# Optimization experiments

Measured on AMD Instinct MI355X. Metric: run time of the kernel, lower is better.

Reference implementation:

```python
import jax, jax.numpy as jnp
import numpy as np


def setup_inputs() -> dict:
    key = jax.random.key(0)
    kq, kk, kv, km = jax.random.split(key, 4)
    B, H, S, D = 1, 16, 2048, 64
    q = jax.random.normal(kq, (B, H, S, D), dtype=jnp.float32)
    k = jax.random.normal(kk, (B, H, S, D), dtype=jnp.float32)
    v = jax.random.normal(kv, (B, H, S, D), dtype=jnp.float32)
    # Boolean attention mask: True = attend, False = ignore.
    # block-pruned use case while keeping the same dense-mask semantics.
    BLK = 64
    tile = jax.random.bernoulli(km, 0.5, (B, H, S // BLK, S // BLK))
    mask = jnp.repeat(jnp.repeat(tile, BLK, axis=2), BLK, axis=3)
    # Guarantee at least something per row is allowed in most rows is not
    # required: fully-masked rows legitimately produce zero output.
    return {"q": q, "k": k, "v": v, "mask": mask}


def reference(q, k, v, mask):
    # Masked scaled-dot-product attention; rows with no valid keys output 0,
    # matching the kernel's `acc / l_i if l_i > 0 else 0` behavior.
    D = q.shape[-1]
    scale = 1.0 / jnp.sqrt(jnp.asarray(D, q.dtype))
    qk = jnp.einsum("bhqd,bhkd->bhqk", q, k) * scale          # [B,H,S,S]
    neg_inf = jnp.asarray(-jnp.inf, qk.dtype)
    s = jnp.where(mask, qk, neg_inf)
    m = jnp.max(s, axis=-1, keepdims=True)                      # row max (may be -inf)
    m_safe = jnp.where(jnp.isfinite(m), m, jnp.zeros_like(m))
    p = jnp.where(mask, jnp.exp(s - m_safe), jnp.zeros_like(qk))  # unnormalized probs
    l = jnp.sum(p, axis=-1, keepdims=True)                      # [B,H,S,1]
    acc = jnp.einsum("bhqk,bhkd->bhqd", p, v)
    out = jnp.where(l > 0, acc / jnp.where(l > 0, l, jnp.ones_like(l)), jnp.zeros_like(acc))
    return out
```

## Files before the change

### kernel.cpp

```cpp
#include <hip/hip_runtime.h>
#include <hip/hip_bf16.h>
#include <stdint.h>

typedef __bf16 bf16;
typedef __attribute__((ext_vector_type(4))) __bf16 bf16x4;
typedef __attribute__((ext_vector_type(8))) __bf16 bf16x8;
typedef __attribute__((ext_vector_type(4))) float f32x4;
typedef __attribute__((ext_vector_type(4))) unsigned int u32x4;

#define NH 16
#define SEQ 2048
#define DH 64
#define NT 32
#define SCALE 0.125f
#define NEGINF (-1e30f)
#define IMG_TILE 8192

#define WS_KIMG  65536
#define WS_VIMG  (WS_KIMG + (size_t)NH * NT * IMG_TILE)
#define WS_NEED  (WS_VIMG + (size_t)NH * NT * IMG_TILE)

__device__ __forceinline__ unsigned swz16(int row, int bytecol) {
  return (unsigned)(row * 128 + (bytecol ^ ((row & 7) << 4)));
}

__global__ void __launch_bounds__(256) conv_kernel(
    const float* __restrict__ kg, const float* __restrict__ vg,
    unsigned char* __restrict__ ws)
{
  const int b = blockIdx.x, tid = threadIdx.x;
  const int h = b & 15, kt = b >> 4, kb = kt << 6;
  unsigned char* kimg = ws + WS_KIMG + (size_t)(h * NT + kt) * IMG_TILE;
  unsigned char* vimg = ws + WS_VIMG + (size_t)(h * NT + kt) * IMG_TILE;
  __shared__ float T[64][65];
  const int row = tid >> 2, c0 = (tid & 3) * 16;

  {
    const f32x4* rp = (const f32x4*)(kg + ((size_t)(h * SEQ) + kb + row) * DH + c0);
    f32x4 a0 = rp[0], a1 = rp[1], a2 = rp[2], a3 = rp[3];
    float* d = &T[row][c0];
    #pragma unroll
    for (int j = 0; j < 4; ++j) {
      d[j] = a0[j]; d[4 + j] = a1[j]; d[8 + j] = a2[j]; d[12 + j] = a3[j];
    }
  }
  __syncthreads();
  #pragma unroll
  for (int i = 0; i < 2; ++i) {
    const int slot = tid + 256 * i, g = slot >> 6, ll = slot & 63;
    const int nd = g >> 1, ks = g & 1;
    const float* s = &T[16 * nd + (ll & 15)][ks * 32 + (ll >> 4) * 8];
    bf16x8 o;
    #pragma unroll
    for (int j = 0; j < 8; ++j) o[j] = (bf16)s[j];
    *(bf16x8*)(kimg + slot * 16) = o;
  }
  __syncthreads();
  {
    const f32x4* rp = (const f32x4*)(vg + ((size_t)(h * SEQ) + kb + row) * DH + c0);
    f32x4 a0 = rp[0], a1 = rp[1], a2 = rp[2], a3 = rp[3];
    float* d = &T[row][c0];
    #pragma unroll
    for (int j = 0; j < 4; ++j) {
      d[j] = a0[j]; d[4 + j] = a1[j]; d[8 + j] = a2[j]; d[12 + j] = a3[j];
    }
  }
  __syncthreads();
  #pragma unroll
  for (int i = 0; i < 2; ++i) {
    const int slot = tid + 256 * i, g = slot >> 6, ll = slot & 63;
    const int nd = g >> 1, ks = g & 1;
    const int r0 = ks * 32 + (ll >> 4) * 8, col = 16 * nd + (ll & 15);
    bf16x8 o;
    #pragma unroll
    for (int j = 0; j < 8; ++j) o[j] = (bf16)T[r0 + j][col];
    *(bf16x8*)(vimg + slot * 16) = o;
  }
}

template<bool IMG>
__global__ void __launch_bounds__(256, 2) fused_attn_kernel(
    const float* __restrict__ qg, const float* __restrict__ kg,
    const float* __restrict__ vg, const void* __restrict__ maskg,
    float* __restrict__ outg, const unsigned char* __restrict__ ws)
{
  const int bid = blockIdx.x;
  const int h = bid & 15, qt = bid >> 4, qb = qt << 6;
  const int tid = threadIdx.x, l = tid & 63, rw = tid >> 6;
  const int qrow = l & 15, kgrp = l >> 4;

  __shared__ __attribute__((aligned(16))) bf16 Pl[4][1024];
  __shared__ unsigned sOr[2][32], sAnd[2][32];
  __shared__ unsigned char tfl[32];
  __shared__ unsigned char Ll[32];
  __shared__ int lcnt;
  __shared__ int clsS;

  bf16x8 qa[2];
  {
    const float* qp = qg + ((size_t)(h * SEQ) + qb + 16 * rw + qrow) * DH;
    #pragma unroll
    for (int ks = 0; ks < 2; ++ks) {
      f32x4 x0 = *(const f32x4*)(qp + ks * 32 + kgrp * 8);
      f32x4 x1 = *(const f32x4*)(qp + ks * 32 + kgrp * 8 + 4);
      bf16x8 a;
      #pragma unroll
      for (int j = 0; j < 4; ++j) {
        a[j] = (bf16)(x0[j] * SCALE); a[4 + j] = (bf16)(x1[j] * SCALE);
      }
      qa[ks] = a;
    }
  }

  if (tid == 0) clsS = 0;
  __syncthreads();
  {
    u32x4 t = ((const u32x4*)maskg)[tid];
    int bits = 0;
    #pragma unroll
    for (int j = 0; j < 4; ++j) {
      if (t[j] == 0x01010101u) bits |= 1;
      else if (t[j] == 1u) bits |= 2;
    }
    const int wb = (__any(bits & 1) ? 1 : 0) | (__any(bits & 2) ? 2 : 0);
    if (l == 0 && wb) atomicOr(&clsS, wb);
  }
  __syncthreads();
  const int byteMode = ((clsS & 1) || !(clsS & 2)) ? 1 : 0;

  const int half = tid >> 7;
  if (byteMode) {
    const unsigned char* rp = (const unsigned char*)maskg
        + ((size_t)(h * SEQ) + qb + half * 63) * SEQ + (tid & 127) * 16;
    u32x4 t = *(const u32x4*)rp;
    unsigned o = t[0] | t[1] | t[2] | t[3];
    unsigned a = t[0] & t[1] & t[2] & t[3];
    o |= __shfl_xor(o, 1); a &= __shfl_xor(a, 1);
    o |= __shfl_xor(o, 2); a &= __shfl_xor(a, 2);
    if ((l & 3) == 0) {
      const int kt = ((tid >> 6) & 1) * 16 + (l >> 2);
      sOr[half][kt] = o; sAnd[half][kt] = a;
    }
  } else {
    const unsigned char* rbase = (const unsigned char*)maskg
        + ((size_t)(h * SEQ) + qb + half * 63) * (size_t)SEQ * 4;
    const int c0 = tid & 127;
    unsigned oo[4], aa[4];
    #pragma unroll
    for (int p = 0; p < 4; ++p) {
      u32x4 t = *(const u32x4*)(rbase + (p * 128 + c0) * 16);
      oo[p] = t[0] | t[1] | t[2] | t[3];
      aa[p] = t[0] & t[1] & t[2] & t[3];
    }
    #pragma unroll
    for (int d = 1; d <= 8; d <<= 1)
      #pragma unroll
      for (int p = 0; p < 4; ++p) {
        oo[p] |= __shfl_xor(oo[p], d); aa[p] &= __shfl_xor(aa[p], d);
      }
    if ((l & 15) == 0) {
      #pragma unroll
      for (int p = 0; p < 4; ++p) {
        const int kt = p * 8 + ((tid >> 6) & 1) * 4 + (l >> 4);
        sOr[half][kt] = oo[p]; sAnd[half][kt] = aa[p];
      }
    }
  }
  __syncthreads();
  if (tid < 32) {
    const int kt = tid;
    const unsigned o0 = sOr[0][kt], a0 = sAnd[0][kt];
    const unsigned o1 = sOr[1][kt], a1 = sAnd[1][kt];
    int active, allT = 0;
    if (o0 == a0 && o1 == a1 && o0 == o1) {
      if (o0 == 0u) active = 0;
      else {
        active = 1;
        allT = byteMode
             ? (((((a0 & 0x7F7F7F7Fu) + 0x7F7F7F7Fu) | a0) & 0x80808080u) == 0x80808080u)
             : 1;
      }
    } else {
      active = ((o0 | o1) != 0u);
    }
    tfl[kt] = (unsigned char)(active | (allT ? 2 : 0));
  }
  __syncthreads();
  if (tid == 0) {
    int n = 0;
    for (int kt = 0; kt < NT; ++kt) {
      const unsigned f = tfl[kt];
      if (f & 1) Ll[n++] = (unsigned char)(kt | ((f & 2) ? 0x80 : 0));
    }
    lcnt = n;
  }
  __syncthreads();
  const int cnt = lcnt;

  f32x4 oacc[4];
  #pragma unroll
  for (int nd = 0; nd < 4; ++nd) oacc[nd] = (f32x4){0.f, 0.f, 0.f, 0.f};
  float mrun = NEGINF, lrun = 0.f;

  auto loadK = [&](bf16x8 (&kf)[8], int kt) {
    if constexpr (IMG) {
      const unsigned char* kp = ws + WS_KIMG + (size_t)(h * NT + kt) * IMG_TILE + l * 16;
      #pragma unroll
      for (int g = 0; g < 8; ++g) kf[g] = *(const bf16x8*)(kp + g * 1024);
    } else {
      const int kb = kt << 6;
      #pragma unroll
      for (int g = 0; g < 8; ++g) {
        const int nd = g >> 1, ks = g & 1;
        const float* kr = kg + ((size_t)(h * SEQ) + kb + 16 * nd + qrow) * DH
                          + ks * 32 + kgrp * 8;
        f32x4 x0 = ((const f32x4*)kr)[0], x1 = ((const f32x4*)kr)[1];
        #pragma unroll
        for (int j = 0; j < 4; ++j) { kf[g][j] = (bf16)x0[j]; kf[g][4 + j] = (bf16)x1[j]; }
      }
    }
  };
  auto loadV = [&](bf16x8 (&vf)[8], int kt) {
    if constexpr (IMG) {
      const unsigned char* vp = ws + WS_VIMG + (size_t)(h * NT + kt) * IMG_TILE + l * 16;
      #pragma unroll
      for (int g = 0; g < 8; ++g) vf[g] = *(const bf16x8*)(vp + g * 1024);
    } else {
      const int kb = kt << 6;
      #pragma unroll
      for (int g = 0; g < 8; ++g) {
        const int nd = g >> 1, ks = g & 1;
        const float* vb = vg + ((size_t)(h * SEQ) + kb + ks * 32 + kgrp * 8) * DH
                          + 16 * nd + qrow;
        #pragma unroll
        for (int j = 0; j < 8; ++j) vf[g][j] = (bf16)vb[j * DH];
      }
    }
  };

  char* pw = (char*)Pl[rw];

  auto doTile = [&](int i, bf16x8 (&kf)[8], bf16x8 (&vf)[8],
                    bf16x8 (&kfN)[8], bf16x8 (&vfN)[8]) {
    const unsigned e = Ll[i];
    const int kt = e & 63;
    const int allT = (e & 0x80u) != 0;
    const int kb = kt << 6;

    if (i + 1 < cnt) {
      const int ktn = Ll[i + 1] & 63;
      loadK(kfN, ktn);
      loadV(vfN, ktn);
    }

    f32x4 sfr[4];
    #pragma unroll
    for (int nd = 0; nd < 4; ++nd) sfr[nd] = (f32x4){0.f, 0.f, 0.f, 0.f};
    __builtin_amdgcn_s_setprio(1);
    #pragma unroll
    for (int nd = 0; nd < 4; ++nd)
      #pragma unroll
      for (int ks = 0; ks < 2; ++ks)
        sfr[nd] = __builtin_amdgcn_mfma_f32_16x16x32_bf16(kf[nd * 2 + ks], qa[ks], sfr[nd], 0, 0, 0);
    __builtin_amdgcn_s_setprio(0);

    if (!allT) {
      const size_t base = ((size_t)(h * SEQ) + qb + 16 * rw + qrow) * SEQ + kb + 4 * kgrp;
      #pragma unroll
      for (int nd = 0; nd < 4; ++nd)
        #pragma unroll
        for (int r = 0; r < 4; ++r) {
          const size_t off = base + 16 * nd + r;
          const bool mv = byteMode ? (((const unsigned char*)maskg)[off] != 0)
                                   : (((const unsigned*)maskg)[off] != 0u);
          if (!mv) sfr[nd][r] = NEGINF;
        }
    }

    float mt;
    {
      f32x4 t0, t1;
      #pragma unroll
      for (int r = 0; r < 4; ++r) {
        t0[r] = fmaxf(sfr[0][r], sfr[1][r]);
        t1[r] = fmaxf(sfr[2][r], sfr[3][r]);
      }
      mt = fmaxf(fmaxf(fmaxf(t0[0], t0[1]), fmaxf(t0[2], t0[3])),
                 fmaxf(fmaxf(t1[0], t1[1]), fmaxf(t1[2], t1[3])));
    }
    mt = fmaxf(mt, __shfl_xor(mt, 16));
    mt = fmaxf(mt, __shfl_xor(mt, 32));
    const float mn = fmaxf(mrun, mt);
    const float fac = __expf(mrun - mn);
    float ls = 0.f;
    bf16x4 pb[4];
    #pragma unroll
    for (int nd = 0; nd < 4; ++nd)
      #pragma unroll
      for (int r = 0; r < 4; ++r) {
        const float p = (sfr[nd][r] > -1e20f) ? __expf(sfr[nd][r] - mn) : 0.f;
        ls += p; pb[nd][r] = (bf16)p;
      }
    ls += __shfl_xor(ls, 16);
    ls += __shfl_xor(ls, 32);
    lrun = lrun * fac + ls;
    mrun = mn;
    #pragma unroll
    for (int nd = 0; nd < 4; ++nd)
      #pragma unroll
      for (int r = 0; r < 4; ++r) oacc[nd][r] *= fac;

    #pragma unroll
    for (int nd = 0; nd < 4; ++nd)
      *(bf16x4*)(pw + swz16(qrow, 32 * nd + 8 * kgrp)) = pb[nd];
    bf16x8 ap[2];
    #pragma unroll
    for (int ks = 0; ks < 2; ++ks)
      ap[ks] = *(const bf16x8*)(pw + swz16(qrow, 64 * ks + 16 * kgrp));

    __builtin_amdgcn_s_setprio(1);
    #pragma unroll
    for (int ks = 0; ks < 2; ++ks)
      #pragma unroll
      for (int nd = 0; nd < 4; ++nd)
        oacc[nd] = __builtin_amdgcn_mfma_f32_16x16x32_bf16(vf[nd * 2 + ks], ap[ks], oacc[nd], 0, 0, 0);
    __builtin_amdgcn_s_setprio(0);
  };

  bf16x8 kfA[8], vfA[8], kfB[8], vfB[8];
  if (cnt > 0) { loadK(kfA, Ll[0] & 63); loadV(vfA, Ll[0] & 63); }

  int i = 0;
  while (i < cnt) {
    doTile(i, kfA, vfA, kfB, vfB); ++i;
    if (i >= cnt) break;
    doTile(i, kfB, vfB, kfA, vfA); ++i;
  }

  {
    const float inv = (lrun > 0.f) ? (1.f / lrun) : 0.f;
    const int grow = qb + 16 * rw + qrow;
    float* op = outg + ((size_t)(h * SEQ) + grow) * DH + 4 * kgrp;
    #pragma unroll
    for (int nd = 0; nd < 4; ++nd) {
      f32x4 o;
      #pragma unroll
      for (int r = 0; r < 4; ++r) o[r] = oacc[nd][r] * inv;
      *(f32x4*)(op + 16 * nd) = o;
    }
  }
}

extern "C" void kernel_launch(void* const* d_in, const int* in_sizes, int n_in,
                              void* d_out, int out_size, void* d_ws, size_t ws_size,
                              hipStream_t stream) {
  const float* q = (const float*)d_in[0];
  const float* k = (const float*)d_in[1];
  const float* v = (const float*)d_in[2];
  const void*  m = d_in[3];
  float* out = (float*)d_out;
  unsigned char* ws = (unsigned char*)d_ws;

  if (ws_size >= WS_NEED) {
    conv_kernel<<<NH * NT, 256, 0, stream>>>(k, v, ws);
    fused_attn_kernel<true><<<NH * NT, 256, 0, stream>>>(q, k, v, m, out, ws);
  } else {
    fused_attn_kernel<false><<<NH * NT, 256, 0, stream>>>(q, k, v, m, out, ws);
  }
}
```

Measured before the change: 39.16 us.

## Split K/V conversion across blocks and shrink prefetch registers for higher occupancy

The conversion kernel now launches twice as many blocks, each converting either a K tile or a V tile, which halves per-block work and adds parallelism. The attention kernel drops the double-buffered K/V register sets. It prefetches only the next K tile after the QK MFMA and loads V just in time, and launch bounds are raised to allow 4 blocks per CU. This cuts register pressure to raise occupancy, at the cost of exposing V load latency that was previously hidden by prefetching.

Measured after the change: 40.10 us. 2.4% more time.

```diff
diff --git a/kernel.cpp b/kernel.cpp
--- a/kernel.cpp
+++ b/kernel.cpp
@@ -29,14 +29,14 @@
     unsigned char* __restrict__ ws)
 {
   const int b = blockIdx.x, tid = threadIdx.x;
-  const int h = b & 15, kt = b >> 4, kb = kt << 6;
-  unsigned char* kimg = ws + WS_KIMG + (size_t)(h * NT + kt) * IMG_TILE;
-  unsigned char* vimg = ws + WS_VIMG + (size_t)(h * NT + kt) * IMG_TILE;
+  const int h = b & 15, kt = (b >> 4) & 31, which = b >> 9;
+  const int kb = kt << 6;
   __shared__ float T[64][65];
   const int row = tid >> 2, c0 = (tid & 3) * 16;
 
+  const float* src = which ? vg : kg;
   {
-    const f32x4* rp = (const f32x4*)(kg + ((size_t)(h * SEQ) + kb + row) * DH + c0);
+    const f32x4* rp = (const f32x4*)(src + ((size_t)(h * SEQ) + kb + row) * DH + c0);
     f32x4 a0 = rp[0], a1 = rp[1], a2 = rp[2], a3 = rp[3];
     float* d = &T[row][c0];
     #pragma unroll
@@ -45,41 +45,35 @@
     }
   }
   __syncthreads();
-  #pragma unroll
-  for (int i = 0; i < 2; ++i) {
-    const int slot = tid + 256 * i, g = slot >> 6, ll = slot & 63;
-    const int nd = g >> 1, ks = g & 1;
-    const float* s = &T[16 * nd + (ll & 15)][ks * 32 + (ll >> 4) * 8];
-    bf16x8 o;
-    #pragma unroll
-    for (int j = 0; j < 8; ++j) o[j] = (bf16)s[j];
-    *(bf16x8*)(kimg + slot * 16) = o;
-  }
-  __syncthreads();
-  {
-    const f32x4* rp = (const f32x4*)(vg + ((size_t)(h * SEQ) + kb + row) * DH + c0);
-    f32x4 a0 = rp[0], a1 = rp[1], a2 = rp[2], a3 = rp[3];
-    float* d = &T[row][c0];
-    #pragma unroll
-    for (int j = 0; j < 4; ++j) {
-      d[j] = a0[j]; d[4 + j] = a1[j]; d[8 + j] = a2[j]; d[12 + j] = a3[j];
-    }
-  }
-  __syncthreads();
-  #pragma unroll
-  for (int i = 0; i < 2; ++i) {
-    const int slot = tid + 256 * i, g = slot >> 6, ll = slot & 63;
-    const int nd = g >> 1, ks = g & 1;
-    const int r0 = ks * 32 + (ll >> 4) * 8, col = 16 * nd + (ll & 15);
-    bf16x8 o;
-    #pragma unroll
-    for (int j = 0; j < 8; ++j) o[j] = (bf16)T[r0 + j][col];
-    *(bf16x8*)(vimg + slot * 16) = o;
+  if (which == 0) {
+    unsigned char* kimg = ws + WS_KIMG + (size_t)(h * NT + kt) * IMG_TILE;
+    #pragma unroll
+    for (int i = 0; i < 2; ++i) {
+      const int slot = tid + 256 * i, g = slot >> 6, ll = slot & 63;
+      const int nd = g >> 1, ks = g & 1;
+      const float* s = &T[16 * nd + (ll & 15)][ks * 32 + (ll >> 4) * 8];
+      bf16x8 o;
+      #pragma unroll
+      for (int j = 0; j < 8; ++j) o[j] = (bf16)s[j];
+      *(bf16x8*)(kimg + slot * 16) = o;
+    }
+  } else {
+    unsigned char* vimg = ws + WS_VIMG + (size_t)(h * NT + kt) * IMG_TILE;
+    #pragma unroll
+    for (int i = 0; i < 2; ++i) {
+      const int slot = tid + 256 * i, g = slot >> 6, ll = slot & 63;
+      const int nd = g >> 1, ks = g & 1;
+      const int r0 = ks * 32 + (ll >> 4) * 8, col = 16 * nd + (ll & 15);
+      bf16x8 o;
+      #pragma unroll
+      for (int j = 0; j < 8; ++j) o[j] = (bf16)T[r0 + j][col];
+      *(bf16x8*)(vimg + slot * 16) = o;
+    }
   }
 }
 
 template<bool IMG>
-__global__ void __launch_bounds__(256, 2) fused_attn_kernel(
+__global__ void __launch_bounds__(256, 4) fused_attn_kernel(
     const float* __restrict__ qg, const float* __restrict__ kg,
     const float* __restrict__ vg, const void* __restrict__ maskg,
     float* __restrict__ outg, const unsigned char* __restrict__ ws)
@@ -220,13 +214,37 @@
       }
     }
   };
-  auto loadV = [&](bf16x8 (&vf)[8], int kt) {
+
+  bf16x8 kf[8];
+  if (cnt > 0) loadK(kf, Ll[0] & 63);
+
+  char* pw = (char*)Pl[rw];
+
+  for (int i = 0; i < cnt; ++i) {
+    const unsigned e = Ll[i];
+    const int kt = e & 63;
+    const int allT = (e & 0x80u) != 0;
+    const int kb = kt << 6;
+
+    f32x4 sfr[4];
+    #pragma unroll
+    for (int nd = 0; nd < 4; ++nd) sfr[nd] = (f32x4){0.f, 0.f, 0.f, 0.f};
+    __builtin_amdgcn_s_setprio(1);
+    #pragma unroll
+    for (int nd = 0; nd < 4; ++nd)
+      #pragma unroll
+      for (int ks = 0; ks < 2; ++ks)
+        sfr[nd] = __builtin_amdgcn_mfma_f32_16x16x32_bf16(kf[nd * 2 + ks], qa[ks], sfr[nd], 0, 0, 0);
+    __builtin_amdgcn_s_setprio(0);
+
+    if (i + 1 < cnt) loadK(kf, Ll[i + 1] & 63);
+
+    bf16x8 vf[8];
     if constexpr (IMG) {
       const unsigned char* vp = ws + WS_VIMG + (size_t)(h * NT + kt) * IMG_TILE + l * 16;
       #pragma unroll
       for (int g = 0; g < 8; ++g) vf[g] = *(const bf16x8*)(vp + g * 1024);
     } else {
-      const int kb = kt << 6;
       #pragma unroll
       for (int g = 0; g < 8; ++g) {
         const int nd = g >> 1, ks = g & 1;
@@ -236,33 +254,6 @@
         for (int j = 0; j < 8; ++j) vf[g][j] = (bf16)vb[j * DH];
       }
     }
-  };
-
-  char* pw = (char*)Pl[rw];
-
-  auto doTile = [&](int i, bf16x8 (&kf)[8], bf16x8 (&vf)[8],
-                    bf16x8 (&kfN)[8], bf16x8 (&vfN)[8]) {
-    const unsigned e = Ll[i];
-    const int kt = e & 63;
-    const int allT = (e & 0x80u) != 0;
-    const int kb = kt << 6;
-
-    if (i + 1 < cnt) {
-      const int ktn = Ll[i + 1] & 63;
-      loadK(kfN, ktn);
-      loadV(vfN, ktn);
-    }
-
-    f32x4 sfr[4];
-    #pragma unroll
-    for (int nd = 0; nd < 4; ++nd) sfr[nd] = (f32x4){0.f, 0.f, 0.f, 0.f};
-    __builtin_amdgcn_s_setprio(1);
-    #pragma unroll
-    for (int nd = 0; nd < 4; ++nd)
-      #pragma unroll
-      for (int ks = 0; ks < 2; ++ks)
-        sfr[nd] = __builtin_amdgcn_mfma_f32_16x16x32_bf16(kf[nd * 2 + ks], qa[ks], sfr[nd], 0, 0, 0);
-    __builtin_amdgcn_s_setprio(0);
 
     if (!allT) {
       const size_t base = ((size_t)(h * SEQ) + qb + 16 * rw + qrow) * SEQ + kb + 4 * kgrp;
@@ -325,16 +316,6 @@
       for (int nd = 0; nd < 4; ++nd)
         oacc[nd] = __builtin_amdgcn_mfma_f32_16x16x32_bf16(vf[nd * 2 + ks], ap[ks], oacc[nd], 0, 0, 0);
     __builtin_amdgcn_s_setprio(0);
-  };
-
-  bf16x8 kfA[8], vfA[8], kfB[8], vfB[8];
-  if (cnt > 0) { loadK(kfA, Ll[0] & 63); loadV(vfA, Ll[0] & 63); }
-
-  int i = 0;
-  while (i < cnt) {
-    doTile(i, kfA, vfA, kfB, vfB); ++i;
-    if (i >= cnt) break;
-    doTile(i, kfB, vfB, kfA, vfA); ++i;
   }
 
   {
@@ -362,7 +343,7 @@
   unsigned char* ws = (unsigned char*)d_ws;
 
   if (ws_size >= WS_NEED) {
-    conv_kernel<<<NH * NT, 256, 0, stream>>>(k, v, ws);
+    conv_kernel<<<2 * NH * NT, 256, 0, stream>>>(k, v, ws);
     fused_attn_kernel<true><<<NH * NT, 256, 0, stream>>>(q, k, v, m, out, ws);
   } else {
     fused_attn_kernel<false><<<NH * NT, 256, 0, stream>>>(q, k, v, m, out, ws);
```
